# Performance work log

Measured on AMD Instinct MI355X. Metric: run time of the kernel, lower is better.

Reference implementation:

```python
import jax, jax.numpy as jnp
import numpy as np

B, L, D = 1, 4096, 1152
N, H = 16, 72            # num_heads, head_dim = d_model // num_heads
S = 64                   # num_patches_side = image_size // patch_size = 896 // 14
BASE = 100.0             # base_frequency for 2D RoPE
EPS = 1e-6


def _rmsnorm(t, scale):
    # t: [..., H]; Gemma-style zero-init scale -> multiply by (1 + scale)
    var = jnp.mean(t * t, axis=-1, keepdims=True)
    t = t * jax.lax.rsqrt(var + EPS)
    if scale is not None:
        t = t * (1.0 + scale)
    return t


def _rope_axis(t, pos):
    # t: [B, L, N, half]; pos: [B, L]. Split-half rotation with given base.
    half = t.shape[-1]
    freqs = BASE ** (-jnp.arange(0, half, 2, dtype=jnp.float32) * 2.0 / half)  # [half//2]
    ang = pos[:, :, None] * freqs                      # [B, L, half//2]
    cos = jnp.cos(ang)[:, :, None, :]
    sin = jnp.sin(ang)[:, :, None, :]
    t1, t2 = t[..., : half // 2], t[..., half // 2 :]
    return jnp.concatenate([t1 * cos - t2 * sin, t1 * sin + t2 * cos], axis=-1)


def _rope_2d(t, rows, cols):
    # first half of head_dim rotated by row position, second half by column position
    h2 = t.shape[-1] // 2
    return jnp.concatenate(
        [_rope_axis(t[..., :h2], rows), _rope_axis(t[..., h2:], cols)], axis=-1
    )


def setup_inputs() -> dict:
    key = jax.random.key(0)
    ks = jax.random.split(key, 5)
    s = 0.02
    return {
        "x": jax.random.normal(ks[0], (B, L, D), dtype=jnp.float32),
        "q_w": jax.random.normal(ks[1], (D, D), dtype=jnp.float32) * s,
        "q_b": jnp.zeros((D,), dtype=jnp.float32),
        "kv_w": jax.random.normal(ks[2], (D, 2 * D), dtype=jnp.float32) * s,
        "kv_b": jnp.zeros((2 * D,), dtype=jnp.float32),
        "o_w": jax.random.normal(ks[3], (D, D), dtype=jnp.float32) * s,
        "o_b": jnp.zeros((D,), dtype=jnp.float32),
        "q_scale": jnp.zeros((H,), dtype=jnp.float32),  # RMSNorm zero_init
        "k_scale": jnp.zeros((H,), dtype=jnp.float32),  # RMSNorm zero_init
    }


def reference(x, q_w, q_b, kv_w, kv_b, o_w, o_b, q_scale, k_scale):
    q = (x @ q_w + q_b).reshape(B, L, N, H)
    kv = (x @ kv_w + kv_b).reshape(B, L, 2, N, H)
    k, v = kv[:, :, 0], kv[:, :, 1]

    q = _rmsnorm(q, q_scale)
    k = _rmsnorm(k, k_scale)
    v = _rmsnorm(v, None)  # with_scale=False

    rows = jnp.repeat(jnp.arange(S, dtype=jnp.float32), S)[None, :L]  # [1, L]
    cols = jnp.tile(jnp.arange(S, dtype=jnp.float32), S)[None, :L]
    rows = jnp.broadcast_to(rows, (B, L))
    cols = jnp.broadcast_to(cols, (B, L))

    q = _rope_2d(q, rows, cols)  # scale = 1.0
    k = _rope_2d(k, rows, cols)

    attn = jnp.einsum("bqnh,bknh->bnqk", q, k)          # [B, N, L, L]
    attn = jax.nn.softmax(attn, axis=-1)
    out = jnp.einsum("bnqk,bknh->bqnh", attn, v).reshape(B, L, D)
    return out @ o_w + o_b
```

## Files before the change

kernel.cpp:

```cpp
#include <hip/hip_runtime.h>
#include <cstdint>
#include <cstddef>

#define LSEQ 4096
#define DMODEL 1152
#define NH 16
#define HD 72
#define HP96 96
#define HP80 80
#define NQKV 3456

typedef unsigned short u16;
typedef unsigned int u32;
typedef __attribute__((ext_vector_type(4))) float f32x4;
typedef __attribute__((ext_vector_type(4))) u32 u32x4;
typedef _Float16 f16x8 __attribute__((ext_vector_type(8), may_alias));
typedef unsigned short us8 __attribute__((ext_vector_type(8), may_alias));
typedef unsigned short us4 __attribute__((ext_vector_type(4), may_alias));

static __device__ __forceinline__ u16 f2h(float f) {
  _Float16 h = (_Float16)f;
  return __builtin_bit_cast(u16, h);
}
static __device__ __forceinline__ float h2f(u16 b) {
  return (float)__builtin_bit_cast(_Float16, b);
}

static __device__ __forceinline__ float fast_exp2(float x) {
#if __has_builtin(__builtin_amdgcn_exp2f)
  return __builtin_amdgcn_exp2f(x);
#else
  float r;
  asm("v_exp_f32 %0, %1" : "=v"(r) : "v"(x));
  return r;
#endif
}

__global__ void k_cvt_f16(const float* __restrict__ src, u16* __restrict__ dst, int n4) {
  int i = blockIdx.x * blockDim.x + threadIdx.x;
  int stride = gridDim.x * blockDim.x;
  for (; i < n4; i += stride) {
    float4 v = ((const float4*)src)[i];
    us4 o; o[0] = f2h(v.x); o[1] = f2h(v.y); o[2] = f2h(v.z); o[3] = f2h(v.w);
    ((us4*)dst)[i] = o;
  }
}

__global__ void k_transp_w(const float* __restrict__ src, u16* __restrict__ dst, int K, int N) {
  __shared__ float tile[32][33];
  int tx = threadIdx.x & 31, ty = threadIdx.x >> 5;
  int n0 = blockIdx.x * 32, k0 = blockIdx.y * 32;
#pragma unroll
  for (int j = 0; j < 4; ++j)
    tile[ty + j * 8][tx] = src[(size_t)(k0 + ty + j * 8) * N + n0 + tx];
  __syncthreads();
#pragma unroll
  for (int j = 0; j < 4; ++j)
    dst[(size_t)(n0 + ty + j * 8) * K + k0 + tx] = f2h(tile[tx][ty + j * 8]);
}

template <bool OUTF32>
__global__ __launch_bounds__(256) void k_gemm_bt(
    const u16* __restrict__ A, const u16* __restrict__ Bt,
    const float* __restrict__ bias, void* __restrict__ Cout,
    int M, int N, int K) {
  __shared__ __align__(16) u16 sA[2][128][40];
  __shared__ __align__(16) u16 sB[2][128][40];
  int t = threadIdx.x;
  int l = t & 63, w = t >> 6, lo = l & 15, hi = l >> 4;
  int m0 = blockIdx.y * 128, n0 = blockIdx.x * 128;
  int wm = (w >> 1) * 64, wn = (w & 1) * 64;
  int sr = t >> 1, sh = (t & 1) * 16;
  const u16* pa = A + (size_t)(m0 + sr) * K + sh;
  const u16* pb = Bt + (size_t)(n0 + sr) * K + sh;
  f32x4 acc[4][4] = {};
  us8 ra0 = *(const us8*)(pa), ra1 = *(const us8*)(pa + 8);
  us8 rb0 = *(const us8*)(pb), rb1 = *(const us8*)(pb + 8);
  int nk = K >> 5;
  for (int ks = 0; ks < nk; ++ks) {
    int buf = ks & 1;
    *(us8*)&sA[buf][sr][sh] = ra0; *(us8*)&sA[buf][sr][sh + 8] = ra1;
    *(us8*)&sB[buf][sr][sh] = rb0; *(us8*)&sB[buf][sr][sh + 8] = rb1;
    if (ks + 1 < nk) {
      int off = (ks + 1) * 32;
      ra0 = *(const us8*)(pa + off); ra1 = *(const us8*)(pa + off + 8);
      rb0 = *(const us8*)(pb + off); rb1 = *(const us8*)(pb + off + 8);
    }
    asm volatile("s_waitcnt lgkmcnt(0)" ::: "memory");
    __builtin_amdgcn_s_barrier();
    f16x8 af[4], bf[4];
#pragma unroll
    for (int mi = 0; mi < 4; ++mi) af[mi] = *(const f16x8*)&sA[buf][wm + mi * 16 + lo][hi * 8];
#pragma unroll
    for (int ni = 0; ni < 4; ++ni) bf[ni] = *(const f16x8*)&sB[buf][wn + ni * 16 + lo][hi * 8];
#pragma unroll
    for (int mi = 0; mi < 4; ++mi)
#pragma unroll
      for (int ni = 0; ni < 4; ++ni)
        acc[mi][ni] = __builtin_amdgcn_mfma_f32_16x16x32_f16(af[mi], bf[ni], acc[mi][ni], 0, 0, 0);
  }
#pragma unroll
  for (int mi = 0; mi < 4; ++mi)
#pragma unroll
    for (int ni = 0; ni < 4; ++ni) {
      int row = m0 + wm + mi * 16 + hi * 4;
      int col = n0 + wn + ni * 16 + lo;
      float bv = bias ? bias[col] : 0.0f;
#pragma unroll
      for (int rr = 0; rr < 4; ++rr) {
        float v = acc[mi][ni][rr] + bv;
        if (OUTF32) ((float*)Cout)[(size_t)(row + rr) * N + col] = v;
        else        ((u16*)Cout)[(size_t)(row + rr) * N + col] = f2h(v);
      }
    }
}

__global__ __launch_bounds__(256) void k_norm_rope(
    const u16* __restrict__ qkv,
    const float* __restrict__ q_b, const float* __restrict__ kv_b,
    const float* __restrict__ q_s, const float* __restrict__ k_s,
    u16* __restrict__ qp, u16* __restrict__ kp, u16* __restrict__ vn) {
  __shared__ float s_q[DMODEL], s_k[DMODEL], s_v[DMODEL];
  __shared__ float cs[4][18];
  int t = threadIdx.x;
  int tok = blockIdx.x;
  if (t < 36) {
    int i = t < 18 ? t : t - 18;
    float f = exp2f(-(float)i * (6.6438561897747247f / 9.0f));
    float pos = (t < 18) ? (float)(tok >> 6) : (float)(tok & 63);
    float s, c;
    sincosf(pos * f, &s, &c);
    if (t < 18) { cs[0][i] = c; cs[1][i] = s; }
    else        { cs[2][i] = c; cs[3][i] = s; }
  }
  const u16* rowp = qkv + (size_t)tok * NQKV;
  for (int c = t; c < NQKV / 8; c += 256) {
    int base8 = c * 8;
    us8 v = *(const us8*)(rowp + base8);
    float* dst; const float* bias; int off;
    if (c < 144)      { dst = s_q; bias = q_b;           off = base8; }
    else if (c < 288) { dst = s_k; bias = kv_b;          off = base8 - DMODEL; }
    else              { dst = s_v; bias = kv_b + DMODEL; off = base8 - 2 * DMODEL; }
#pragma unroll
    for (int j = 0; j < 8; ++j) dst[off + j] = h2f(v[j]) + bias[off + j];
  }
  __syncthreads();
  int h = t >> 4, sub = t & 15;
  int base = h * HD;
  float aq = 0, ak = 0, av = 0;
#pragma unroll
  for (int j = 0; j < 5; ++j) {
    int idx = sub + 16 * j;
    if (idx < HD) {
      float a = s_q[base + idx], b = s_k[base + idx], c = s_v[base + idx];
      aq += a * a; ak += b * b; av += c * c;
    }
  }
#pragma unroll
  for (int m = 1; m <= 8; m <<= 1) {
    aq += __shfl_xor(aq, m, 64);
    ak += __shfl_xor(ak, m, 64);
    av += __shfl_xor(av, m, 64);
  }
  float rq = rsqrtf(aq / 72.f + 1e-6f);
  float rk = rsqrtf(ak / 72.f + 1e-6f);
  float rv = rsqrtf(av / 72.f + 1e-6f);
  size_t ob96 = ((size_t)h * LSEQ + tok) * HP96;
  size_t ob80 = ((size_t)h * LSEQ + tok) * HP80;
#pragma unroll
  for (int j = 0; j < 6; ++j) {
    int idx = sub + 16 * j;
    float oq = 0.f, ok = 0.f;
    if (idx < HD) {
      int sec = idx >= 36;
      int loc = idx - sec * 36;
      int i = loc >= 18 ? loc - 18 : loc;
      float c = cs[sec * 2 + 0][i], s = cs[sec * 2 + 1][i];
      int p1 = sec * 36 + i, p2 = p1 + 18;
      float q1 = s_q[base + p1] * rq * (1.f + q_s[p1]);
      float q2 = s_q[base + p2] * rq * (1.f + q_s[p2]);
      float k1 = s_k[base + p1] * rk * (1.f + k_s[p1]);
      float k2 = s_k[base + p2] * rk * (1.f + k_s[p2]);
      if (loc < 18) { oq = q1 * c - q2 * s; ok = k1 * c - k2 * s; }
      else          { oq = q1 * s + q2 * c; ok = k1 * s + k2 * c; }
    }
    qp[ob96 + idx] = f2h(oq);
    kp[ob96 + idx] = f2h(ok);
  }
#pragma unroll
  for (int j = 0; j < 5; ++j) {
    int idx = sub + 16 * j;
    float ov = (idx < HD) ? s_v[base + idx] * rv : (idx == 72 ? 1.0f : 0.f);
    vn[ob80 + idx] = f2h(ov);
  }
}

__global__ __launch_bounds__(256) void k_vfrag(const u16* __restrict__ vn, u16* __restrict__ vf) {
  __shared__ u16 tl[32][84];
  int head = blockIdx.y, kb = blockIdx.x;
  int t = threadIdx.x;
  const u16* src = vn + ((size_t)head * LSEQ + kb * 32) * HP80;
  for (int p = t; p < 32 * 20; p += 256) {
    int rr = p / 20, c4 = p % 20;
    *(us4*)&tl[rr][c4 * 4] = *(const us4*)(src + rr * HP80 + c4 * 4);
  }
  __syncthreads();
  u16* dst = vf + ((size_t)head * 128 + kb) * 2560;
  for (int u = t; u < 320; u += 256) {
    int ht = u >> 6, ll = u & 63, lo2 = ll & 15, hi2 = ll >> 4;
    us8 o;
#pragma unroll
    for (int j = 0; j < 8; ++j)
      o[j] = tl[(j >> 2) * 16 + hi2 * 4 + (j & 3)][ht * 16 + lo2];
    *(us8*)&dst[(size_t)u * 8] = o;
  }
}

__global__ __launch_bounds__(256, 2) void k_flash(
    const u16* __restrict__ qp, const u16* __restrict__ kp,
    const u16* __restrict__ vf, u16* __restrict__ pbuf, float2* __restrict__ dmb) {
  __shared__ __align__(16) u16 sK[2][64][104];
  int t = threadIdx.x;
  int l = t & 63, w = t >> 6, lo = l & 15, hi = l >> 4;
  int id = blockIdx.x, r = id >> 3;
  int half = r & 1, qb = (r >> 1) & 31, head = ((r >> 6) << 3) + (id & 7);
  const float L2E = 1.4426950408889634f;

  const u16* qbase = qp + ((size_t)head * LSEQ + qb * 128 + w * 32 + lo) * HP96 + hi * 8;
  f16x8 qf[2][3];
#pragma unroll
  for (int g = 0; g < 2; ++g)
#pragma unroll
    for (int c = 0; c < 3; ++c)
      qf[g][c] = *(const f16x8*)(qbase + g * 16 * HP96 + c * 32);

  f32x4 oacc[2][5] = {};
  float mrun[2];
#pragma unroll
  for (int g = 0; g < 2; ++g) mrun[g] = -__builtin_inff();

  int sr_ = t >> 2, sq4 = (t & 3) * 24;
  const u16* kptr = kp + ((size_t)head * LSEQ + half * 2048 + sr_) * HP96 + sq4;
  us8 kx0 = *(const us8*)(kptr), kx1 = *(const us8*)(kptr + 8), kx2 = *(const us8*)(kptr + 16);

  const u16* vptr = vf + ((size_t)head * 128 + half * 64) * 2560 + (size_t)l * 8;
  us8 vA[5], vB[5];
#pragma unroll
  for (int ht = 0; ht < 5; ++ht) vA[ht] = *(const us8*)(vptr + ht * 512);
  vptr += 2560;

  for (int kt = 0; kt < 32; ++kt) {
    u16* skb = &sK[kt & 1][0][0];
    *(us8*)(skb + sr_ * 104 + sq4) = kx0;
    *(us8*)(skb + sr_ * 104 + sq4 + 8) = kx1;
    *(us8*)(skb + sr_ * 104 + sq4 + 16) = kx2;
    if (kt < 31) {
      kx0 = *(const us8*)(kptr + 6144);
      kx1 = *(const us8*)(kptr + 6144 + 8);
      kx2 = *(const us8*)(kptr + 6144 + 16);
      kptr += 6144;
    }
    asm volatile("s_waitcnt lgkmcnt(0)" ::: "memory");
    __builtin_amdgcn_s_barrier();
    const u16(*sKb)[104] = (const u16(*)[104])skb;
    f32x4 sacc[2][4] = {};
#pragma unroll
    for (int c = 0; c < 3; ++c)
#pragma unroll
      for (int nt = 0; nt < 4; ++nt) {
        f16x8 bk = *(const f16x8*)&sKb[lo + 16 * nt][c * 32 + hi * 8];
#pragma unroll
        for (int g = 0; g < 2; ++g)
          sacc[g][nt] = __builtin_amdgcn_mfma_f32_16x16x32_f16(bk, qf[g][c], sacc[g][nt], 0, 0, 0);
      }
    float mt[2];
#pragma unroll
    for (int g = 0; g < 2; ++g) {
      float m = fmaxf(fmaxf(fmaxf(sacc[g][0][0], sacc[g][0][1]), sacc[g][0][2]), sacc[g][0][3]);
#pragma unroll
      for (int nt = 1; nt < 4; ++nt)
        m = fmaxf(m, fmaxf(fmaxf(fmaxf(sacc[g][nt][0], sacc[g][nt][1]), sacc[g][nt][2]), sacc[g][nt][3]));
      m = fmaxf(m, __shfl_xor(m, 16, 64));
      m = fmaxf(m, __shfl_xor(m, 32, 64));
      mt[g] = m;
    }
    bool need = (mt[0] > mrun[0] + 8.f) | (mt[1] > mrun[1] + 8.f);
    if (__any(need)) {
#pragma unroll
      for (int g = 0; g < 2; ++g) {
        float mn = fmaxf(mrun[g], mt[g]);
        float al = fast_exp2((mrun[g] - mn) * L2E);
        mrun[g] = mn;
#pragma unroll
        for (int ht = 0; ht < 5; ++ht)
#pragma unroll
          for (int rr = 0; rr < 4; ++rr) oacc[g][ht][rr] *= al;
      }
    }
#pragma unroll
    for (int kc = 0; kc < 2; ++kc) {
#pragma unroll
      for (int ht = 0; ht < 5; ++ht) vB[ht] = *(const us8*)(vptr + ht * 512);
      vptr += 2560;
#pragma unroll
      for (int g = 0; g < 2; ++g) {
        float nm = -mrun[g] * L2E;
        float p0[4], p1[4];
#pragma unroll
        for (int rr = 0; rr < 4; ++rr) {
          p0[rr] = fast_exp2(__builtin_fmaf(sacc[g][2 * kc][rr], L2E, nm));
          p1[rr] = fast_exp2(__builtin_fmaf(sacc[g][2 * kc + 1][rr], L2E, nm));
        }
        u32x4 pw = {__builtin_bit_cast(u32, __builtin_amdgcn_cvt_pkrtz(p0[0], p0[1])),
                    __builtin_bit_cast(u32, __builtin_amdgcn_cvt_pkrtz(p0[2], p0[3])),
                    __builtin_bit_cast(u32, __builtin_amdgcn_cvt_pkrtz(p1[0], p1[1])),
                    __builtin_bit_cast(u32, __builtin_amdgcn_cvt_pkrtz(p1[2], p1[3]))};
        f16x8 pb = __builtin_bit_cast(f16x8, pw);
#pragma unroll
        for (int ht = 0; ht < 5; ++ht)
          oacc[g][ht] = __builtin_amdgcn_mfma_f32_16x16x32_f16(
              __builtin_bit_cast(f16x8, vA[ht]), pb, oacc[g][ht], 0, 0, 0);
      }
#pragma unroll
      for (int ht = 0; ht < 5; ++ht) vA[ht] = vB[ht];
    }
  }
#pragma unroll
  for (int g = 0; g < 2; ++g) {
    float den = __shfl(oacc[g][4][0], lo + 32, 64);
    float inv = 1.f / den;
    int row = qb * 128 + w * 32 + g * 16 + lo;
    u16* orow = pbuf + ((size_t)half * LSEQ + row) * DMODEL + head * HD;
#pragma unroll
    for (int ht = 0; ht < 5; ++ht)
#pragma unroll
      for (int rr = 0; rr < 4; ++rr) {
        int h = 16 * ht + 4 * hi + rr;
        if (h < HD) orow[h] = f2h(oacc[g][ht][rr] * inv);
      }
    if (hi == 0) {
      float2 dm; dm.x = den; dm.y = mrun[g];
      dmb[((size_t)half * NH + head) * LSEQ + row] = dm;
    }
  }
}

__global__ __launch_bounds__(384) void k_combine(
    const u16* __restrict__ pbuf, const float2* __restrict__ dmb, u16* __restrict__ attb) {
  const float L2E = 1.4426950408889634f;
  int tok = blockIdx.x, t = threadIdx.x;
  for (int c = t; c < DMODEL; c += 384) {
    int head = c / HD;
    float2 dm0 = dmb[(size_t)head * LSEQ + tok];
    float2 dm1 = dmb[((size_t)NH + head) * LSEQ + tok];
    float M = fmaxf(dm0.y, dm1.y);
    float w0 = dm0.x * fast_exp2((dm0.y - M) * L2E);
    float w1 = dm1.x * fast_exp2((dm1.y - M) * L2E);
    float o0 = h2f(pbuf[(size_t)tok * DMODEL + c]);
    float o1 = h2f(pbuf[((size_t)LSEQ + tok) * DMODEL + c]);
    attb[(size_t)tok * DMODEL + c] = f2h((w0 * o0 + w1 * o1) / (w0 + w1));
  }
}

extern "C" void kernel_launch(void* const* d_in, const int* in_sizes, int n_in,
                              void* d_out, int out_size, void* d_ws, size_t ws_size,
                              hipStream_t stream) {
  const float* x    = (const float*)d_in[0];
  const float* q_w  = (const float*)d_in[1];
  const float* q_b  = (const float*)d_in[2];
  const float* kv_w = (const float*)d_in[3];
  const float* kv_b = (const float*)d_in[4];
  const float* o_w  = (const float*)d_in[5];
  const float* o_b  = (const float*)d_in[6];
  const float* q_s  = (const float*)d_in[7];
  const float* k_s  = (const float*)d_in[8];
  char* ws = (char*)d_ws;
  u16* xb   = (u16*)(ws + 0);
  u16* wT   = (u16*)(ws + 9437184);
  u16* oT   = (u16*)(ws + 17399808);
  u16* qkvb = (u16*)(ws + 20054016);
  u16* qp   = (u16*)(ws + 48365568);
  u16* kp   = (u16*)(ws + 60948480);
  u16* vn   = (u16*)(ws + 73531392);
  u16* vfb  = (u16*)(ws + 0);
  float2* dmb = (float2*)(ws + 10485760);
  u16* attb = (u16*)(ws + 20054016);
  u16* pbuf = (u16*)(ws + 29491200);

  k_cvt_f16<<<2048, 256, 0, stream>>>(x, xb, LSEQ * DMODEL / 4);
  k_transp_w<<<dim3(36, 36), 256, 0, stream>>>(q_w, wT, DMODEL, DMODEL);
  k_transp_w<<<dim3(72, 36), 256, 0, stream>>>(kv_w, wT + (size_t)DMODEL * DMODEL, DMODEL, 2 * DMODEL);
  k_transp_w<<<dim3(36, 36), 256, 0, stream>>>(o_w, oT, DMODEL, DMODEL);
  k_gemm_bt<false><<<dim3(27, 32), 256, 0, stream>>>(xb, wT, nullptr, qkvb, LSEQ, NQKV, DMODEL);
  k_norm_rope<<<LSEQ, 256, 0, stream>>>(qkvb, q_b, kv_b, q_s, k_s, qp, kp, vn);
  k_vfrag<<<dim3(128, 16), 256, 0, stream>>>(vn, vfb);
  k_flash<<<1024, 256, 0, stream>>>(qp, kp, vfb, pbuf, dmb);
  k_combine<<<LSEQ, 384, 0, stream>>>(pbuf, dmb, attb);
  k_gemm_bt<true><<<dim3(9, 32), 256, 0, stream>>>(attb, oT, o_b, (float*)d_out, LSEQ, DMODEL, DMODEL);
}
```

Baseline: 250.7 us.

## Fuse fp32-to-fp16 input conversion into QKV GEMM and remap workgroups XCD-aware

Drops the separate x-to-fp16 conversion kernel. The QKV GEMM now loads fp32 A tiles directly and converts them while staging into LDS. Both GEMMs also switch to a 1D grid with a workgroup-id swizzle that spreads consecutive IDs across the 8 XCDs, aiming for better L2 locality. This removes one launch and one round trip of x through memory, at the cost of twice the A-load bytes per tile inside the GEMM and extra conversion ALU work there.

```diff
diff --git a/kernel.cpp b/kernel.cpp
--- a/kernel.cpp
+++ b/kernel.cpp
@@ -36,16 +36,6 @@
 #endif
 }
 
-__global__ void k_cvt_f16(const float* __restrict__ src, u16* __restrict__ dst, int n4) {
-  int i = blockIdx.x * blockDim.x + threadIdx.x;
-  int stride = gridDim.x * blockDim.x;
-  for (; i < n4; i += stride) {
-    float4 v = ((const float4*)src)[i];
-    us4 o; o[0] = f2h(v.x); o[1] = f2h(v.y); o[2] = f2h(v.z); o[3] = f2h(v.w);
-    ((us4*)dst)[i] = o;
-  }
-}
-
 __global__ void k_transp_w(const float* __restrict__ src, u16* __restrict__ dst, int K, int N) {
   __shared__ float tile[32][33];
   int tx = threadIdx.x & 31, ty = threadIdx.x >> 5;
@@ -59,31 +49,59 @@
     dst[(size_t)(n0 + ty + j * 8) * K + k0 + tx] = f2h(tile[tx][ty + j * 8]);
 }
 
-template <bool OUTF32>
+template <bool OUTF32, bool AF32>
 __global__ __launch_bounds__(256) void k_gemm_bt(
-    const u16* __restrict__ A, const u16* __restrict__ Bt,
+    const void* __restrict__ Av, const u16* __restrict__ Bt,
     const float* __restrict__ bias, void* __restrict__ Cout,
-    int M, int N, int K) {
+    int M, int N, int K, int nbx, int nwg) {
   __shared__ __align__(16) u16 sA[2][128][40];
   __shared__ __align__(16) u16 sB[2][128][40];
   int t = threadIdx.x;
   int l = t & 63, w = t >> 6, lo = l & 15, hi = l >> 4;
-  int m0 = blockIdx.y * 128, n0 = blockIdx.x * 128;
+  int wg = blockIdx.x;
+  int wgid = (wg & 7) * (nwg >> 3) + (wg >> 3);
+  int bx = wgid % nbx, by = wgid / nbx;
+  int m0 = by * 128, n0 = bx * 128;
   int wm = (w >> 1) * 64, wn = (w & 1) * 64;
   int sr = t >> 1, sh = (t & 1) * 16;
-  const u16* pa = A + (size_t)(m0 + sr) * K + sh;
   const u16* pb = Bt + (size_t)(n0 + sr) * K + sh;
   f32x4 acc[4][4] = {};
-  us8 ra0 = *(const us8*)(pa), ra1 = *(const us8*)(pa + 8);
+  us8 ra0, ra1;
+  float4 fa0, fa1, fa2, fa3;
+  const u16* pa16 = nullptr;
+  const float* pa32 = nullptr;
+  if (AF32) {
+    pa32 = (const float*)Av + (size_t)(m0 + sr) * K + sh;
+    fa0 = *(const float4*)(pa32);      fa1 = *(const float4*)(pa32 + 4);
+    fa2 = *(const float4*)(pa32 + 8);  fa3 = *(const float4*)(pa32 + 12);
+  } else {
+    pa16 = (const u16*)Av + (size_t)(m0 + sr) * K + sh;
+    ra0 = *(const us8*)(pa16); ra1 = *(const us8*)(pa16 + 8);
+  }
   us8 rb0 = *(const us8*)(pb), rb1 = *(const us8*)(pb + 8);
   int nk = K >> 5;
   for (int ks = 0; ks < nk; ++ks) {
     int buf = ks & 1;
-    *(us8*)&sA[buf][sr][sh] = ra0; *(us8*)&sA[buf][sr][sh + 8] = ra1;
+    if (AF32) {
+      us8 c0, c1;
+#pragma unroll
+      for (int j = 0; j < 4; ++j) {
+        c0[j] = f2h(fa0[j]); c0[4 + j] = f2h(fa1[j]);
+        c1[j] = f2h(fa2[j]); c1[4 + j] = f2h(fa3[j]);
+      }
+      *(us8*)&sA[buf][sr][sh] = c0; *(us8*)&sA[buf][sr][sh + 8] = c1;
+    } else {
+      *(us8*)&sA[buf][sr][sh] = ra0; *(us8*)&sA[buf][sr][sh + 8] = ra1;
+    }
     *(us8*)&sB[buf][sr][sh] = rb0; *(us8*)&sB[buf][sr][sh + 8] = rb1;
     if (ks + 1 < nk) {
       int off = (ks + 1) * 32;
-      ra0 = *(const us8*)(pa + off); ra1 = *(const us8*)(pa + off + 8);
+      if (AF32) {
+        fa0 = *(const float4*)(pa32 + off);      fa1 = *(const float4*)(pa32 + off + 4);
+        fa2 = *(const float4*)(pa32 + off + 8);  fa3 = *(const float4*)(pa32 + off + 12);
+      } else {
+        ra0 = *(const us8*)(pa16 + off); ra1 = *(const us8*)(pa16 + off + 8);
+      }
       rb0 = *(const us8*)(pb + off); rb1 = *(const us8*)(pb + off + 8);
     }
     asm volatile("s_waitcnt lgkmcnt(0)" ::: "memory");
@@ -375,7 +393,6 @@
   const float* q_s  = (const float*)d_in[7];
   const float* k_s  = (const float*)d_in[8];
   char* ws = (char*)d_ws;
-  u16* xb   = (u16*)(ws + 0);
   u16* wT   = (u16*)(ws + 9437184);
   u16* oT   = (u16*)(ws + 17399808);
   u16* qkvb = (u16*)(ws + 20054016);
@@ -387,14 +404,15 @@
   u16* attb = (u16*)(ws + 20054016);
   u16* pbuf = (u16*)(ws + 29491200);
 
-  k_cvt_f16<<<2048, 256, 0, stream>>>(x, xb, LSEQ * DMODEL / 4);
   k_transp_w<<<dim3(36, 36), 256, 0, stream>>>(q_w, wT, DMODEL, DMODEL);
   k_transp_w<<<dim3(72, 36), 256, 0, stream>>>(kv_w, wT + (size_t)DMODEL * DMODEL, DMODEL, 2 * DMODEL);
   k_transp_w<<<dim3(36, 36), 256, 0, stream>>>(o_w, oT, DMODEL, DMODEL);
-  k_gemm_bt<false><<<dim3(27, 32), 256, 0, stream>>>(xb, wT, nullptr, qkvb, LSEQ, NQKV, DMODEL);
+  k_gemm_bt<false, true><<<864, 256, 0, stream>>>(x, wT, nullptr, qkvb,
+                                                  LSEQ, NQKV, DMODEL, 27, 864);
   k_norm_rope<<<LSEQ, 256, 0, stream>>>(qkvb, q_b, kv_b, q_s, k_s, qp, kp, vn);
   k_vfrag<<<dim3(128, 16), 256, 0, stream>>>(vn, vfb);
   k_flash<<<1024, 256, 0, stream>>>(qp, kp, vfb, pbuf, dmb);
   k_combine<<<LSEQ, 384, 0, stream>>>(pbuf, dmb, attb);
-  k_gemm_bt<true><<<dim3(9, 32), 256, 0, stream>>>(attb, oT, o_b, (float*)d_out, LSEQ, DMODEL, DMODEL);
-}
+  k_gemm_bt<true, false><<<288, 256, 0, stream>>>(attb, oT, o_b, (float*)d_out,
+                                                  LSEQ, DMODEL, DMODEL, 9, 288);
+}
```

Measured after the change: 249.0 us (median of 2 runs). Within noise of the previous version (-0.7%).
